# Performance work log

Hardware: AMD Instinct MI355X
Metric: run time of the kernel (lower is better)

Reference implementation:

```python
import jax, jax.numpy as jnp
import numpy as np

N_ATOM = 10000
D = 256
N_EDGE = 160000
BN_EPS = 1e-6


def _bn_eval(x, g, b, m, v):
    # BatchNorm1d in eval mode
    return (x - m) * jax.lax.rsqrt(v + BN_EPS) * g + b


def setup_inputs() -> dict:
    key = jax.random.key(0)
    ks = jax.random.split(key, 12)
    def glorot(k, shape):
        fan_in = shape[-1]
        return jax.random.normal(k, shape, dtype=jnp.float32) / np.sqrt(fan_in)
    inp = {
        'atom': jax.random.normal(ks[0], (N_ATOM, D), dtype=jnp.float32),
        'bond_index': jax.random.randint(ks[1], (2, N_EDGE), 0, N_ATOM, dtype=jnp.int32),
        # align: Linear(2D -> 1) + BN(1)
        'W_align': glorot(ks[2], (1, 2 * D)),
        'b_align': jnp.zeros((1,), jnp.float32),
        'bn_a_g': jnp.ones((1,), jnp.float32),
        'bn_a_b': jnp.zeros((1,), jnp.float32),
        'bn_a_m': jnp.zeros((1,), jnp.float32),
        'bn_a_v': jnp.ones((1,), jnp.float32),
        # attend: Linear(D -> D) + BN(D)
        'W_att': glorot(ks[3], (D, D)),
        'b_att': jnp.zeros((D,), jnp.float32),
        'bn_t_g': jnp.ones((D,), jnp.float32),
        'bn_t_b': jnp.zeros((D,), jnp.float32),
        'bn_t_m': jnp.zeros((D,), jnp.float32),
        'bn_t_v': jnp.ones((D,), jnp.float32),
        # GRUCell(D, D): weights stacked [r; z; n] as in torch
        'W_ih': glorot(ks[4], (3 * D, D)),
        'W_hh': glorot(ks[5], (3 * D, D)),
        'b_ih': jnp.zeros((3 * D,), jnp.float32),
        'b_hh': jnp.zeros((3 * D,), jnp.float32),
    }
    return inp


def reference(atom, bond_index, W_align, b_align, bn_a_g, bn_a_b, bn_a_m, bn_a_v,
              W_att, b_att, bn_t_g, bn_t_b, bn_t_m, bn_t_v,
              W_ih, W_hh, b_ih, b_hh):
    num_atom = atom.shape[0]
    src = bond_index[0]
    dst = bond_index[1]

    # gather + concat: [E, 2D]
    feat_align = jnp.concatenate([atom[src], atom[dst]], axis=-1)
    # align score: Linear(2D->1) + BN + leaky_relu -> [E, 1]
    s = feat_align @ W_align.T + b_align
    s = _bn_eval(s, bn_a_g, bn_a_b, bn_a_m, bn_a_v)
    s = jax.nn.leaky_relu(s, negative_slope=0.01)

    # segment softmax over edges grouped by src atom
    seg_max = jax.ops.segment_max(s, src, num_segments=num_atom)  # [N, 1]
    e = jnp.exp(s - seg_max[src])
    denom = jax.ops.segment_sum(e, src, num_segments=num_atom)    # [N, 1]
    attn = e / (denom[src] + 1e-8)                                # [E, 1]

    # attend: Linear(D->D) + BN on gathered dst features
    h = atom[dst] @ W_att.T + b_att
    h = _bn_eval(h, bn_t_g, bn_t_b, bn_t_m, bn_t_v)

    # weighted scatter-add aggregation -> [N, D], then ELU
    context = jax.ops.segment_sum(attn * h, src, num_segments=num_atom)
    context = jax.nn.elu(context)

    # GRUCell: input=context, hidden=atom
    gi = context @ W_ih.T + b_ih   # [N, 3D]
    gh = atom @ W_hh.T + b_hh      # [N, 3D]
    i_r, i_z, i_n = jnp.split(gi, 3, axis=-1)
    h_r, h_z, h_n = jnp.split(gh, 3, axis=-1)
    r = jax.nn.sigmoid(i_r + h_r)
    z = jax.nn.sigmoid(i_z + h_z)
    n = jnp.tanh(i_n + r * h_n)
    update = (1.0 - z) * n + z * atom
    return update
```

## Files before the change

kernel.cpp:

```cpp
#include <hip/hip_runtime.h>
#include <hip/hip_bf16.h>

#define D 256
#define CAP 64

typedef __attribute__((ext_vector_type(8))) short bf16x8;
typedef __attribute__((ext_vector_type(4))) short s16x4;
typedef __attribute__((ext_vector_type(4))) float f32x4;

#define MFMA __builtin_amdgcn_mfma_f32_16x16x32_bf16

__device__ __forceinline__ float s2f(short u) {
    union { unsigned int i; float f; } c;
    c.i = ((unsigned int)(unsigned short)u) << 16;
    return c.f;
}
__device__ __forceinline__ short f2s(float f) {
    union { float f; unsigned int u; } c; c.f = f;
    unsigned int u = c.u;
    u += 0x7fffu + ((u >> 16) & 1u);
    return (short)(u >> 16);
}
__device__ __forceinline__ void ld16_lds(void* lds, const void* gsrc) {
    __builtin_amdgcn_global_load_lds(
        (const __attribute__((address_space(1))) unsigned int*)gsrc,
        (__attribute__((address_space(3))) unsigned int*)lds,
        16, 0, 0);
}

__global__ __launch_bounds__(256) void prep_kernel(
    const float* __restrict__ atom, short* __restrict__ atom_bf,
    const float* __restrict__ W_align, const float* __restrict__ b_align,
    const float* __restrict__ g, const float* __restrict__ bb,
    const float* __restrict__ mn, const float* __restrict__ vr,
    float* __restrict__ p0p, float* __restrict__ p1p,
    const float* __restrict__ Wa, short* __restrict__ Wa_bf,
    const float* __restrict__ Wi, short* __restrict__ Wi_bf,
    const float* __restrict__ Wh, short* __restrict__ Wh_bf,
    int* __restrict__ cnt,
    int N, int NROWB, int WCVTB)
{
    int b = blockIdx.x, tid = threadIdx.x;
    if (b < NROWB) {
        int wave = tid >> 6, lane = tid & 63;
        int row = b * 4 + wave;
        if (row >= N) return;
        float4 a = *(const float4*)(atom + (size_t)row * D + lane * 4);
        s16x4 o; o[0] = f2s(a.x); o[1] = f2s(a.y); o[2] = f2s(a.z); o[3] = f2s(a.w);
        ((s16x4*)(atom_bf + (size_t)row * D))[lane] = o;
        float4 w0 = *(const float4*)(W_align + lane * 4);
        float4 w1 = *(const float4*)(W_align + D + lane * 4);
        float d0 = a.x * w0.x + a.y * w0.y + a.z * w0.z + a.w * w0.w;
        float d1 = a.x * w1.x + a.y * w1.y + a.z * w1.z + a.w * w1.w;
        #pragma unroll
        for (int s = 32; s > 0; s >>= 1) {
            d0 += __shfl_xor(d0, s, 64);
            d1 += __shfl_xor(d1, s, 64);
        }
        if (lane == 0) {
            float A = rsqrtf(vr[0] + 1e-6f) * g[0];
            p0p[row] = A * (d0 + b_align[0]) + bb[0] - A * mn[0];
            p1p[row] = A * d1;
        }
        return;
    }
    b -= NROWB;
    if (b < WCVTB) {
        int nW4 = D * D / 4, nG4 = 3 * D * D / 4;
        int j = b * 256 + tid;
        const float* srcp; short* dstp;
        if (j < nW4) { srcp = Wa; dstp = Wa_bf; }
        else { j -= nW4;
            if (j < nG4) { srcp = Wi; dstp = Wi_bf; }
            else { j -= nG4;
                if (j < nG4) { srcp = Wh; dstp = Wh_bf; }
                else return;
            }
        }
        float4 v = ((const float4*)srcp)[j];
        s16x4 o; o[0] = f2s(v.x); o[1] = f2s(v.y); o[2] = f2s(v.z); o[3] = f2s(v.w);
        ((s16x4*)dstp)[j] = o;
        return;
    }
    b -= WCVTB;
    int i = b * 256 + tid;
    if (i < N) cnt[i] = 0;
}

__global__ __launch_bounds__(256) void fill_hA_kernel(
    const int* __restrict__ src, const int* __restrict__ dst,
    int* __restrict__ cnt, int* __restrict__ dlist, int E, int EB,
    const short* __restrict__ atom_bf, const short* __restrict__ W_bf,
    const float* __restrict__ bias,
    const float* __restrict__ g, const float* __restrict__ bb,
    const float* __restrict__ mn, const float* __restrict__ vr,
    short* __restrict__ hA, int N, int NB)
{
    int tid = threadIdx.x;
    if ((int)blockIdx.x < EB) {
        int e = blockIdx.x * 256 + tid;
        if (e < E) {
            int s = src[e];
            int p = atomicAdd(&cnt[s], 1);
            if (p < CAP) dlist[(s << 6) + p] = dst[e];
        }
        return;
    }
    __shared__ short Bs[2048 * 8];
    int bi = blockIdx.x - EB;
    int xcd = bi & 7, rest = bi >> 3;
    int cb = rest & 3, gh = rest >> 2;
    int gg = gh * 8 + xcd;
    if (gg >= NB) return;
    int c0 = cb * 64;
    #pragma unroll
    for (int it = 0; it < 8; it++) {
        int c = tid + it * 256;
        int l15c = c & 15, quadc = (c >> 4) & 3, t2 = c >> 6;
        int kkc = t2 & 7, jc = t2 >> 3;
        ld16_lds(&Bs[c * 8],
                 W_bf + (size_t)(c0 + jc * 16 + l15c) * D + quadc * 8 + kkc * 32);
    }
    __syncthreads();

    int wave = tid >> 6, lane = tid & 63;
    int quad = lane >> 4, l15 = lane & 15;
    int m0 = gg * 128 + wave * 16;
    int ar0 = m0 + l15;       if (ar0 > N - 1) ar0 = N - 1;
    int ar1 = m0 + 64 + l15;  if (ar1 > N - 1) ar1 = N - 1;
    const short* ap0 = atom_bf + (size_t)ar0 * D + quad * 8;
    const short* ap1 = atom_bf + (size_t)ar1 * D + quad * 8;
    const short* lb = &Bs[lane * 8];
    f32x4 acc[2][4];
    #pragma unroll
    for (int t = 0; t < 2; t++)
        #pragma unroll
        for (int j = 0; j < 4; j++) acc[t][j] = (f32x4){0,0,0,0};
    #pragma unroll
    for (int kk = 0; kk < 8; kk++) {
        int k = kk * 32;
        bf16x8 a0 = *(const bf16x8*)(ap0 + k);
        bf16x8 a1 = *(const bf16x8*)(ap1 + k);
        bf16x8 b0 = *(const bf16x8*)(lb + (0 * 8 + kk) * 512);
        bf16x8 b1 = *(const bf16x8*)(lb + (1 * 8 + kk) * 512);
        bf16x8 b2 = *(const bf16x8*)(lb + (2 * 8 + kk) * 512);
        bf16x8 b3 = *(const bf16x8*)(lb + (3 * 8 + kk) * 512);
        acc[0][0] = MFMA(a0, b0, acc[0][0], 0, 0, 0);
        acc[0][1] = MFMA(a0, b1, acc[0][1], 0, 0, 0);
        acc[0][2] = MFMA(a0, b2, acc[0][2], 0, 0, 0);
        acc[0][3] = MFMA(a0, b3, acc[0][3], 0, 0, 0);
        acc[1][0] = MFMA(a1, b0, acc[1][0], 0, 0, 0);
        acc[1][1] = MFMA(a1, b1, acc[1][1], 0, 0, 0);
        acc[1][2] = MFMA(a1, b2, acc[1][2], 0, 0, 0);
        acc[1][3] = MFMA(a1, b3, acc[1][3], 0, 0, 0);
    }
    #pragma unroll
    for (int j = 0; j < 4; j++) {
        int col = c0 + j * 16 + l15;
        float sc = rsqrtf(vr[col] + 1e-6f) * g[col];
        float sh = bb[col] - mn[col] * sc;
        float bi_ = bias[col];
        #pragma unroll
        for (int t = 0; t < 2; t++) {
            #pragma unroll
            for (int r = 0; r < 4; r++) {
                int row = m0 + t * 64 + quad * 4 + r;
                if (row < N) hA[(size_t)row * D + col] = f2s((acc[t][j][r] + bi_) * sc + sh);
            }
        }
    }
}

__global__ __launch_bounds__(256) void agg_kernel(
    const int* __restrict__ cnt, const int* __restrict__ dlist,
    const float* __restrict__ p0p, const float* __restrict__ p1p,
    const short* __restrict__ hA, short* __restrict__ ctx, int N)
{
    int w = (blockIdx.x * blockDim.x + threadIdx.x) >> 6;
    int lane = threadIdx.x & 63;
    if (w >= N) return;
    int deg = cnt[w]; if (deg > CAP) deg = CAP;
    int base = w << 6;
    int d = 0; float e = 0.f;
    if (lane < deg) {
        d = dlist[base + lane];
        float x = p0p[w] + p1p[d];
        x = x > 0.f ? x : 0.01f * x;
        e = __expf(x);
    }
    float se = e;
    #pragma unroll
    for (int s = 32; s > 0; s >>= 1) se += __shfl_xor(se, s, 64);

    int grp = lane >> 4, l16 = lane & 15;
    float acc[16];
    #pragma unroll
    for (int i = 0; i < 16; i++) acc[i] = 0.f;
    int nit = (deg + 3) >> 2;
    for (int it = 0; it < nit; ++it) {
        int j = it * 4 + grp;
        int jc = j < deg ? j : 0;
        int dj = __shfl(d, jc, 64);
        float ej = __shfl(e, jc, 64);
        if (j >= deg) ej = 0.f;
        const short* hp = hA + (size_t)dj * D + l16 * 16;
        bf16x8 h0 = *(const bf16x8*)(hp);
        bf16x8 h1 = *(const bf16x8*)(hp + 8);
        #pragma unroll
        for (int i = 0; i < 8; i++) acc[i]     += ej * s2f(h0[i]);
        #pragma unroll
        for (int i = 0; i < 8; i++) acc[8 + i] += ej * s2f(h1[i]);
    }
    #pragma unroll
    for (int i = 0; i < 16; i++) {
        acc[i] += __shfl_xor(acc[i], 16, 64);
        acc[i] += __shfl_xor(acc[i], 32, 64);
    }
    if (grp == 0) {
        float inv = 1.f / (se + 1e-8f);
        bf16x8 o0, o1;
        #pragma unroll
        for (int i = 0; i < 8; i++) {
            float v0 = acc[i] * inv;
            v0 = v0 > 0.f ? v0 : __expf(v0) - 1.f;
            o0[i] = f2s(v0);
            float v1 = acc[8 + i] * inv;
            v1 = v1 > 0.f ? v1 : __expf(v1) - 1.f;
            o1[i] = f2s(v1);
        }
        short* cp = ctx + (size_t)w * D + l16 * 16;
        *(bf16x8*)cp = o0;
        *(bf16x8*)(cp + 8) = o1;
    }
}

__global__ __launch_bounds__(256) void gru_kernel(
    const short* __restrict__ ctx, const short* __restrict__ atom_bf,
    const short* __restrict__ W_ih, const short* __restrict__ W_hh,
    const float* __restrict__ b_ih, const float* __restrict__ b_hh,
    float* __restrict__ out, int N, int NB)
{
    __shared__ short Bs[3072 * 8];
    int bi = blockIdx.x;
    int xcd = bi & 7, rest = bi >> 3;
    int cb = rest & 15, gh = rest >> 4;
    int gg = gh * 8 + xcd;
    if (gg >= NB) return;
    int c0 = cb * 16;
    int tid = threadIdx.x;

    int wave = tid >> 6, lane = tid & 63;
    int quad = lane >> 4, l15 = lane & 15;
    int m0 = gg * 128 + wave * 16;
    int ar0 = m0 + l15;       if (ar0 > N - 1) ar0 = N - 1;
    int ar1 = m0 + 64 + l15;  if (ar1 > N - 1) ar1 = N - 1;
    const short* cp0 = ctx + (size_t)ar0 * D + quad * 8;
    const short* ap0 = atom_bf + (size_t)ar0 * D + quad * 8;
    const short* cp1 = ctx + (size_t)ar1 * D + quad * 8;
    const short* ap1 = atom_bf + (size_t)ar1 * D + quad * 8;

    bf16x8 c0v = *(const bf16x8*)(cp0);
    bf16x8 a0v = *(const bf16x8*)(ap0);
    bf16x8 c1v = *(const bf16x8*)(cp1);
    bf16x8 a1v = *(const bf16x8*)(ap1);

    #pragma unroll
    for (int it = 0; it < 12; it++) {
        int c = tid + it * 256;
        int l15c = c & 15, quadc = (c >> 4) & 3, t2 = c >> 6;
        int kkc = t2 & 7, gate = t2 >> 3;
        const short* srcp = (gate < 3)
            ? W_ih + (size_t)(gate * 256 + c0 + l15c) * D + quadc * 8 + kkc * 32
            : W_hh + (size_t)((gate - 3) * 256 + c0 + l15c) * D + quadc * 8 + kkc * 32;
        ld16_lds(&Bs[c * 8], srcp);
    }
    __syncthreads();

    const short* lb = &Bs[lane * 8];
    f32x4 gi[2][3], gh_[2][3];
    #pragma unroll
    for (int t = 0; t < 2; t++)
        #pragma unroll
        for (int j = 0; j < 3; j++) { gi[t][j] = (f32x4){0,0,0,0}; gh_[t][j] = (f32x4){0,0,0,0}; }
    #pragma unroll
    for (int kk = 0; kk < 8; kk++) {
        bf16x8 nc0, na0, nc1, na1;
        if (kk < 7) {
            int k = (kk + 1) * 32;
            nc0 = *(const bf16x8*)(cp0 + k);
            na0 = *(const bf16x8*)(ap0 + k);
            nc1 = *(const bf16x8*)(cp1 + k);
            na1 = *(const bf16x8*)(ap1 + k);
        }
        bf16x8 bir = *(const bf16x8*)(lb + (0 * 8 + kk) * 512);
        bf16x8 biz = *(const bf16x8*)(lb + (1 * 8 + kk) * 512);
        bf16x8 bin = *(const bf16x8*)(lb + (2 * 8 + kk) * 512);
        bf16x8 bhr = *(const bf16x8*)(lb + (3 * 8 + kk) * 512);
        bf16x8 bhz = *(const bf16x8*)(lb + (4 * 8 + kk) * 512);
        bf16x8 bhn = *(const bf16x8*)(lb + (5 * 8 + kk) * 512);
        gi[0][0] = MFMA(c0v, bir, gi[0][0], 0, 0, 0);
        gi[0][1] = MFMA(c0v, biz, gi[0][1], 0, 0, 0);
        gi[0][2] = MFMA(c0v, bin, gi[0][2], 0, 0, 0);
        gh_[0][0] = MFMA(a0v, bhr, gh_[0][0], 0, 0, 0);
        gh_[0][1] = MFMA(a0v, bhz, gh_[0][1], 0, 0, 0);
        gh_[0][2] = MFMA(a0v, bhn, gh_[0][2], 0, 0, 0);
        gi[1][0] = MFMA(c1v, bir, gi[1][0], 0, 0, 0);
        gi[1][1] = MFMA(c1v, biz, gi[1][1], 0, 0, 0);
        gi[1][2] = MFMA(c1v, bin, gi[1][2], 0, 0, 0);
        gh_[1][0] = MFMA(a1v, bhr, gh_[1][0], 0, 0, 0);
        gh_[1][1] = MFMA(a1v, bhz, gh_[1][1], 0, 0, 0);
        gh_[1][2] = MFMA(a1v, bhn, gh_[1][2], 0, 0, 0);
        if (kk < 7) { c0v = nc0; a0v = na0; c1v = nc1; a1v = na1; }
    }
    int col = c0 + l15;
    float bir_s = b_ih[col], biz_s = b_ih[col + 256], bin_s = b_ih[col + 512];
    float bhr_s = b_hh[col], bhz_s = b_hh[col + 256], bhn_s = b_hh[col + 512];
    #pragma unroll
    for (int t = 0; t < 2; t++) {
        #pragma unroll
        for (int r = 0; r < 4; r++) {
            int row = m0 + t * 64 + quad * 4 + r;
            if (row < N) {
                float rr = 1.f / (1.f + __expf(-(gi[t][0][r] + bir_s + gh_[t][0][r] + bhr_s)));
                float zz = 1.f / (1.f + __expf(-(gi[t][1][r] + biz_s + gh_[t][1][r] + bhz_s)));
                float nn = tanhf(gi[t][2][r] + bin_s + rr * (gh_[t][2][r] + bhn_s));
                float at = s2f(atom_bf[(size_t)row * D + col]);
                out[(size_t)row * D + col] = (1.f - zz) * nn + zz * at;
            }
        }
    }
}

extern "C" void kernel_launch(void* const* d_in, const int* in_sizes, int n_in,
                              void* d_out, int out_size, void* d_ws, size_t ws_size,
                              hipStream_t stream) {
    const float* atom    = (const float*)d_in[0];
    const int*   bond    = (const int*)d_in[1];
    const float* W_align = (const float*)d_in[2];
    const float* b_align = (const float*)d_in[3];
    const float* bn_a_g  = (const float*)d_in[4];
    const float* bn_a_b  = (const float*)d_in[5];
    const float* bn_a_m  = (const float*)d_in[6];
    const float* bn_a_v  = (const float*)d_in[7];
    const float* W_att   = (const float*)d_in[8];
    const float* b_att   = (const float*)d_in[9];
    const float* bn_t_g  = (const float*)d_in[10];
    const float* bn_t_b  = (const float*)d_in[11];
    const float* bn_t_m  = (const float*)d_in[12];
    const float* bn_t_v  = (const float*)d_in[13];
    const float* W_ih    = (const float*)d_in[14];
    const float* W_hh    = (const float*)d_in[15];
    const float* b_ih    = (const float*)d_in[16];
    const float* b_hh    = (const float*)d_in[17];

    int N = in_sizes[0] / D;
    int E = in_sizes[1] / 2;
    const int* src = bond;
    const int* dst = bond + E;

    char* w = (char*)d_ws;
    size_t o = 0;
    auto alloc = [&](size_t bytes) {
        void* p = w + o;
        o = (o + bytes + 255) & ~(size_t)255;
        return p;
    };
    int*   cnt     = (int*)alloc((size_t)N * 4);
    int*   dlist   = (int*)alloc((size_t)N * CAP * 4);
    float* p0p     = (float*)alloc((size_t)N * 4);
    float* p1p     = (float*)alloc((size_t)N * 4);
    short* hA      = (short*)alloc((size_t)N * D * 2);
    short* ctx     = (short*)alloc((size_t)N * D * 2);
    short* atom_bf = (short*)alloc((size_t)N * D * 2);
    short* Watt_bf = (short*)alloc((size_t)D * D * 2);
    short* Wih_bf  = (short*)alloc((size_t)3 * D * D * 2);
    short* Whh_bf  = (short*)alloc((size_t)3 * D * D * 2);

    int NROWB = (N + 3) / 4;
    int nWtot4 = (D * D + 2 * 3 * D * D) / 4;
    int WCVTB = (nWtot4 + 255) / 256;
    int ZB = (N + 255) / 256;
    int EB = (E + 255) / 256;
    int NB = (N + 127) / 128;
    int GH = (NB + 7) / 8;

    prep_kernel<<<NROWB + WCVTB + ZB, 256, 0, stream>>>(
        atom, atom_bf, W_align, b_align, bn_a_g, bn_a_b, bn_a_m, bn_a_v, p0p, p1p,
        W_att, Watt_bf, W_ih, Wih_bf, W_hh, Whh_bf, cnt, N, NROWB, WCVTB);
    fill_hA_kernel<<<EB + 8 * 4 * GH, 256, 0, stream>>>(
        src, dst, cnt, dlist, E, EB,
        atom_bf, Watt_bf, b_att, bn_t_g, bn_t_b, bn_t_m, bn_t_v, hA, N, NB);
    agg_kernel<<<((size_t)N * 64 + 255) / 256, 256, 0, stream>>>(
        cnt, dlist, p0p, p1p, hA, ctx, N);
    gru_kernel<<<8 * 16 * GH, 256, 0, stream>>>(
        ctx, atom_bf, Wih_bf, Whh_bf, b_ih, b_hh, (float*)d_out, N, NB);
}
```

Measured before the change: 164.9 us.

## Merge prep and hA GEMM into one kernel with inline fp32-to-bf16 conversion

Combines the preparation kernel and the edge-fill/hA GEMM kernel into a single launch. The attention GEMM now reads fp32 atom and W_att directly and converts them to bf16 in registers, which removes the dependency on a prior conversion pass. The count array is zeroed with a memset instead of a block range. This saves one kernel launch and the serialization between the two stages, at the cost of more global traffic (fp32 reads) and VALU conversion work inside the GEMM. It also drops the XCD-aware block swizzle.

```diff
diff --git a/kernel.cpp b/kernel.cpp
--- a/kernel.cpp
+++ b/kernel.cpp
@@ -21,6 +21,14 @@
     u += 0x7fffu + ((u >> 16) & 1u);
     return (short)(u >> 16);
 }
+__device__ __forceinline__ bf16x8 cvt8(const float* p) {
+    float4 f0 = *(const float4*)p;
+    float4 f1 = *(const float4*)(p + 4);
+    bf16x8 r;
+    r[0] = f2s(f0.x); r[1] = f2s(f0.y); r[2] = f2s(f0.z); r[3] = f2s(f0.w);
+    r[4] = f2s(f1.x); r[5] = f2s(f1.y); r[6] = f2s(f1.z); r[7] = f2s(f1.w);
+    return r;
+}
 __device__ __forceinline__ void ld16_lds(void* lds, const void* gsrc) {
     __builtin_amdgcn_global_load_lds(
         (const __attribute__((address_space(1))) unsigned int*)gsrc,
@@ -28,20 +36,97 @@
         16, 0, 0);
 }
 
-__global__ __launch_bounds__(256) void prep_kernel(
-    const float* __restrict__ atom, short* __restrict__ atom_bf,
+__global__ __launch_bounds__(256) void k1_kernel(
+    const float* __restrict__ atom,
+    const float* __restrict__ W_att, const float* __restrict__ bias,
+    const float* __restrict__ g_t, const float* __restrict__ bb_t,
+    const float* __restrict__ mn_t, const float* __restrict__ vr_t,
+    short* __restrict__ hA,
+    const int* __restrict__ src, const int* __restrict__ dst,
+    int* __restrict__ cnt, int* __restrict__ dlist,
     const float* __restrict__ W_align, const float* __restrict__ b_align,
-    const float* __restrict__ g, const float* __restrict__ bb,
-    const float* __restrict__ mn, const float* __restrict__ vr,
+    const float* __restrict__ g_a, const float* __restrict__ bb_a,
+    const float* __restrict__ mn_a, const float* __restrict__ vr_a,
     float* __restrict__ p0p, float* __restrict__ p1p,
-    const float* __restrict__ Wa, short* __restrict__ Wa_bf,
+    short* __restrict__ atom_bf,
     const float* __restrict__ Wi, short* __restrict__ Wi_bf,
     const float* __restrict__ Wh, short* __restrict__ Wh_bf,
-    int* __restrict__ cnt,
-    int N, int NROWB, int WCVTB)
+    int N, int E, int NB, int HB, int FB, int PB)
 {
-    int b = blockIdx.x, tid = threadIdx.x;
-    if (b < NROWB) {
+    int tid = threadIdx.x;
+    int b = blockIdx.x;
+    if (b < HB) {
+        __shared__ short Bs[2048 * 8];
+        int cb = b & 3, gg = b >> 2;
+        if (gg >= NB) return;
+        int c0 = cb * 64;
+        for (int c = tid; c < 2048; c += 256) {
+            int l15c = c & 15, quadc = (c >> 4) & 3, t2 = c >> 6;
+            int kkc = t2 & 7, jc = t2 >> 3;
+            *(bf16x8*)(&Bs[c * 8]) =
+                cvt8(W_att + (size_t)(c0 + jc * 16 + l15c) * D + quadc * 8 + kkc * 32);
+        }
+        __syncthreads();
+
+        int wave = tid >> 6, lane = tid & 63;
+        int quad = lane >> 4, l15 = lane & 15;
+        int m0 = gg * 128 + wave * 16;
+        int ar0 = m0 + l15;       if (ar0 > N - 1) ar0 = N - 1;
+        int ar1 = m0 + 64 + l15;  if (ar1 > N - 1) ar1 = N - 1;
+        const float* ap0 = atom + (size_t)ar0 * D + quad * 8;
+        const float* ap1 = atom + (size_t)ar1 * D + quad * 8;
+        const short* lb = &Bs[lane * 8];
+        f32x4 acc[2][4];
+        #pragma unroll
+        for (int t = 0; t < 2; t++)
+            #pragma unroll
+            for (int j = 0; j < 4; j++) acc[t][j] = (f32x4){0,0,0,0};
+        #pragma unroll
+        for (int kk = 0; kk < 8; kk++) {
+            bf16x8 a0 = cvt8(ap0 + kk * 32);
+            bf16x8 a1 = cvt8(ap1 + kk * 32);
+            bf16x8 b0 = *(const bf16x8*)(lb + (0 * 8 + kk) * 512);
+            bf16x8 b1 = *(const bf16x8*)(lb + (1 * 8 + kk) * 512);
+            bf16x8 b2 = *(const bf16x8*)(lb + (2 * 8 + kk) * 512);
+            bf16x8 b3 = *(const bf16x8*)(lb + (3 * 8 + kk) * 512);
+            acc[0][0] = MFMA(a0, b0, acc[0][0], 0, 0, 0);
+            acc[0][1] = MFMA(a0, b1, acc[0][1], 0, 0, 0);
+            acc[0][2] = MFMA(a0, b2, acc[0][2], 0, 0, 0);
+            acc[0][3] = MFMA(a0, b3, acc[0][3], 0, 0, 0);
+            acc[1][0] = MFMA(a1, b0, acc[1][0], 0, 0, 0);
+            acc[1][1] = MFMA(a1, b1, acc[1][1], 0, 0, 0);
+            acc[1][2] = MFMA(a1, b2, acc[1][2], 0, 0, 0);
+            acc[1][3] = MFMA(a1, b3, acc[1][3], 0, 0, 0);
+        }
+        #pragma unroll
+        for (int j = 0; j < 4; j++) {
+            int col = c0 + j * 16 + l15;
+            float sc = rsqrtf(vr_t[col] + 1e-6f) * g_t[col];
+            float sh = bb_t[col] - mn_t[col] * sc;
+            float bi_ = bias[col];
+            #pragma unroll
+            for (int t = 0; t < 2; t++) {
+                #pragma unroll
+                for (int r = 0; r < 4; r++) {
+                    int row = m0 + t * 64 + quad * 4 + r;
+                    if (row < N) hA[(size_t)row * D + col] = f2s((acc[t][j][r] + bi_) * sc + sh);
+                }
+            }
+        }
+        return;
+    }
+    b -= HB;
+    if (b < FB) {
+        int e = b * 256 + tid;
+        if (e < E) {
+            int s = src[e];
+            int p = atomicAdd(&cnt[s], 1);
+            if (p < CAP) dlist[(s << 6) + p] = dst[e];
+        }
+        return;
+    }
+    b -= FB;
+    if (b < PB) {
         int wave = tid >> 6, lane = tid & 63;
         int row = b * 4 + wave;
         if (row >= N) return;
@@ -58,116 +143,22 @@
             d1 += __shfl_xor(d1, s, 64);
         }
         if (lane == 0) {
-            float A = rsqrtf(vr[0] + 1e-6f) * g[0];
-            p0p[row] = A * (d0 + b_align[0]) + bb[0] - A * mn[0];
+            float A = rsqrtf(vr_a[0] + 1e-6f) * g_a[0];
+            p0p[row] = A * (d0 + b_align[0]) + bb_a[0] - A * mn_a[0];
             p1p[row] = A * d1;
         }
         return;
     }
-    b -= NROWB;
-    if (b < WCVTB) {
-        int nW4 = D * D / 4, nG4 = 3 * D * D / 4;
+    b -= PB;
+    {
+        int nG4 = 3 * D * D / 4;
         int j = b * 256 + tid;
         const float* srcp; short* dstp;
-        if (j < nW4) { srcp = Wa; dstp = Wa_bf; }
-        else { j -= nW4;
-            if (j < nG4) { srcp = Wi; dstp = Wi_bf; }
-            else { j -= nG4;
-                if (j < nG4) { srcp = Wh; dstp = Wh_bf; }
-                else return;
-            }
-        }
+        if (j < nG4) { srcp = Wi; dstp = Wi_bf; }
+        else { j -= nG4; if (j >= nG4) return; srcp = Wh; dstp = Wh_bf; }
         float4 v = ((const float4*)srcp)[j];
         s16x4 o; o[0] = f2s(v.x); o[1] = f2s(v.y); o[2] = f2s(v.z); o[3] = f2s(v.w);
         ((s16x4*)dstp)[j] = o;
-        return;
-    }
-    b -= WCVTB;
-    int i = b * 256 + tid;
-    if (i < N) cnt[i] = 0;
-}
-
-__global__ __launch_bounds__(256) void fill_hA_kernel(
-    const int* __restrict__ src, const int* __restrict__ dst,
-    int* __restrict__ cnt, int* __restrict__ dlist, int E, int EB,
-    const short* __restrict__ atom_bf, const short* __restrict__ W_bf,
-    const float* __restrict__ bias,
-    const float* __restrict__ g, const float* __restrict__ bb,
-    const float* __restrict__ mn, const float* __restrict__ vr,
-    short* __restrict__ hA, int N, int NB)
-{
-    int tid = threadIdx.x;
-    if ((int)blockIdx.x < EB) {
-        int e = blockIdx.x * 256 + tid;
-        if (e < E) {
-            int s = src[e];
-            int p = atomicAdd(&cnt[s], 1);
-            if (p < CAP) dlist[(s << 6) + p] = dst[e];
-        }
-        return;
-    }
-    __shared__ short Bs[2048 * 8];
-    int bi = blockIdx.x - EB;
-    int xcd = bi & 7, rest = bi >> 3;
-    int cb = rest & 3, gh = rest >> 2;
-    int gg = gh * 8 + xcd;
-    if (gg >= NB) return;
-    int c0 = cb * 64;
-    #pragma unroll
-    for (int it = 0; it < 8; it++) {
-        int c = tid + it * 256;
-        int l15c = c & 15, quadc = (c >> 4) & 3, t2 = c >> 6;
-        int kkc = t2 & 7, jc = t2 >> 3;
-        ld16_lds(&Bs[c * 8],
-                 W_bf + (size_t)(c0 + jc * 16 + l15c) * D + quadc * 8 + kkc * 32);
-    }
-    __syncthreads();
-
-    int wave = tid >> 6, lane = tid & 63;
-    int quad = lane >> 4, l15 = lane & 15;
-    int m0 = gg * 128 + wave * 16;
-    int ar0 = m0 + l15;       if (ar0 > N - 1) ar0 = N - 1;
-    int ar1 = m0 + 64 + l15;  if (ar1 > N - 1) ar1 = N - 1;
-    const short* ap0 = atom_bf + (size_t)ar0 * D + quad * 8;
-    const short* ap1 = atom_bf + (size_t)ar1 * D + quad * 8;
-    const short* lb = &Bs[lane * 8];
-    f32x4 acc[2][4];
-    #pragma unroll
-    for (int t = 0; t < 2; t++)
-        #pragma unroll
-        for (int j = 0; j < 4; j++) acc[t][j] = (f32x4){0,0,0,0};
-    #pragma unroll
-    for (int kk = 0; kk < 8; kk++) {
-        int k = kk * 32;
-        bf16x8 a0 = *(const bf16x8*)(ap0 + k);
-        bf16x8 a1 = *(const bf16x8*)(ap1 + k);
-        bf16x8 b0 = *(const bf16x8*)(lb + (0 * 8 + kk) * 512);
-        bf16x8 b1 = *(const bf16x8*)(lb + (1 * 8 + kk) * 512);
-        bf16x8 b2 = *(const bf16x8*)(lb + (2 * 8 + kk) * 512);
-        bf16x8 b3 = *(const bf16x8*)(lb + (3 * 8 + kk) * 512);
-        acc[0][0] = MFMA(a0, b0, acc[0][0], 0, 0, 0);
-        acc[0][1] = MFMA(a0, b1, acc[0][1], 0, 0, 0);
-        acc[0][2] = MFMA(a0, b2, acc[0][2], 0, 0, 0);
-        acc[0][3] = MFMA(a0, b3, acc[0][3], 0, 0, 0);
-        acc[1][0] = MFMA(a1, b0, acc[1][0], 0, 0, 0);
-        acc[1][1] = MFMA(a1, b1, acc[1][1], 0, 0, 0);
-        acc[1][2] = MFMA(a1, b2, acc[1][2], 0, 0, 0);
-        acc[1][3] = MFMA(a1, b3, acc[1][3], 0, 0, 0);
-    }
-    #pragma unroll
-    for (int j = 0; j < 4; j++) {
-        int col = c0 + j * 16 + l15;
-        float sc = rsqrtf(vr[col] + 1e-6f) * g[col];
-        float sh = bb[col] - mn[col] * sc;
-        float bi_ = bias[col];
-        #pragma unroll
-        for (int t = 0; t < 2; t++) {
-            #pragma unroll
-            for (int r = 0; r < 4; r++) {
-                int row = m0 + t * 64 + quad * 4 + r;
-                if (row < N) hA[(size_t)row * D + col] = f2s((acc[t][j][r] + bi_) * sc + sh);
-            }
-        }
     }
 }
 
@@ -372,24 +363,23 @@
     short* hA      = (short*)alloc((size_t)N * D * 2);
     short* ctx     = (short*)alloc((size_t)N * D * 2);
     short* atom_bf = (short*)alloc((size_t)N * D * 2);
-    short* Watt_bf = (short*)alloc((size_t)D * D * 2);
     short* Wih_bf  = (short*)alloc((size_t)3 * D * D * 2);
     short* Whh_bf  = (short*)alloc((size_t)3 * D * D * 2);
 
-    int NROWB = (N + 3) / 4;
-    int nWtot4 = (D * D + 2 * 3 * D * D) / 4;
-    int WCVTB = (nWtot4 + 255) / 256;
-    int ZB = (N + 255) / 256;
-    int EB = (E + 255) / 256;
     int NB = (N + 127) / 128;
     int GH = (NB + 7) / 8;
-
-    prep_kernel<<<NROWB + WCVTB + ZB, 256, 0, stream>>>(
-        atom, atom_bf, W_align, b_align, bn_a_g, bn_a_b, bn_a_m, bn_a_v, p0p, p1p,
-        W_att, Watt_bf, W_ih, Wih_bf, W_hh, Whh_bf, cnt, N, NROWB, WCVTB);
-    fill_hA_kernel<<<EB + 8 * 4 * GH, 256, 0, stream>>>(
-        src, dst, cnt, dlist, E, EB,
-        atom_bf, Watt_bf, b_att, bn_t_g, bn_t_b, bn_t_m, bn_t_v, hA, N, NB);
+    int HB = 4 * NB;
+    int FB = (E + 255) / 256;
+    int PB = (N + 3) / 4;
+    int WB = (2 * 3 * D * D / 4 + 255) / 256;
+
+    hipMemsetAsync(cnt, 0, (size_t)N * 4, stream);
+    k1_kernel<<<HB + FB + PB + WB, 256, 0, stream>>>(
+        atom, W_att, b_att, bn_t_g, bn_t_b, bn_t_m, bn_t_v, hA,
+        src, dst, cnt, dlist,
+        W_align, b_align, bn_a_g, bn_a_b, bn_a_m, bn_a_v, p0p, p1p,
+        atom_bf, W_ih, Wih_bf, W_hh, Whh_bf,
+        N, E, NB, HB, FB, PB);
     agg_kernel<<<((size_t)N * 64 + 255) / 256, 256, 0, stream>>>(
         cnt, dlist, p0p, p1p, hA, ctx, N);
     gru_kernel<<<8 * 16 * GH, 256, 0, stream>>>(
```

Result: no change. 167.7 us (+1.7%).
